# Optimization experiments

Measured on AMD Instinct MI355X. Metric: run time of the kernel, lower is better.

## Reference

```python
import jax, jax.numpy as jnp
import numpy as np

B, T, D, H = 512, 200, 64, 256
C1, C2, C3, R1 = 1024, 256, 10, 1024

def _lin(k, out_d, in_d):
    k1, k2 = jax.random.split(k)
    lim = 1.0 / np.sqrt(in_d)
    w = jax.random.uniform(k1, (out_d, in_d), minval=-lim, maxval=lim, dtype=jnp.float32)
    b = jax.random.uniform(k2, (out_d,), minval=-lim, maxval=lim, dtype=jnp.float32)
    return w, b

def setup_inputs() -> dict:
    key = jax.random.key(0)
    ks = jax.random.split(key, 12)
    lim = 1.0 / np.sqrt(H)
    u = lambda k, sh: jax.random.uniform(k, sh, minval=-lim, maxval=lim, dtype=jnp.float32)
    inp = {"x": jax.random.normal(ks[0], (B, T, D), dtype=jnp.float32)}
    # LSTM layer 0 (input dim D) and layer 1 (input dim H); torch gate order i,f,g,o
    inp["W_ih0"], inp["b_ih0"], inp["b_hh0"] = u(ks[1], (4 * H, D)), u(ks[2], (4 * H,)), u(ks[3], (4 * H,))
    inp["W_ih1"], inp["b_ih1"], inp["b_hh1"] = u(ks[4], (4 * H, H)), u(ks[5], (4 * H,)), u(ks[6], (4 * H,))
    inp["fc1_w"], inp["fc1_b"] = _lin(ks[7], C1, H * T)
    inp["fc2_w"], inp["fc2_b"] = _lin(ks[8], C2, C1)
    inp["fc3_w"], inp["fc3_b"] = _lin(ks[9], C3, C2)
    inp["fc4_w"], inp["fc4_b"] = _lin(ks[10], R1, H * T)
    inp["fc5_w"], inp["fc5_b"] = _lin(ks[11], T, R1)
    return inp

def _lstm_step_zero(x, W_ih, b_ih, b_hh):
    # Single LSTM cell step from h0=c0=0, applied independently to every
    # (batch, timestep) position: gates = x @ W_ih^T + b_ih + b_hh
    gates = jnp.einsum('btd,gd->btg', x, W_ih) + b_ih + b_hh  # [B,T,4H]
    i, f, g, o = jnp.split(gates, 4, axis=-1)  # torch gate order i,f,g,o
    c = jax.nn.sigmoid(i) * jnp.tanh(g)        # c0 = 0 => forget gate irrelevant
    return jax.nn.sigmoid(o) * jnp.tanh(c)

def reference(x, W_ih0, b_ih0, b_hh0, W_ih1, b_ih1, b_hh1,
              fc1_w, fc1_b, fc2_w, fc2_b, fc3_w, fc3_b,
              fc4_w, fc4_b, fc5_w, fc5_b):
    h0 = _lstm_step_zero(x, W_ih0, b_ih0, b_hh0)          # [B,T,H]
    out_total = _lstm_step_zero(h0, W_ih1, b_ih1, b_hh1)  # [B,T,H]
    flat = out_total.reshape(-1, H * T)
    # classification head (dropout = identity in eval)
    c = jax.nn.relu(flat @ fc1_w.T + fc1_b)
    c = jax.nn.relu(c @ fc2_w.T + fc2_b)
    output_class3 = c @ fc3_w.T + fc3_b                   # [B,C3]
    r = jax.nn.relu(flat @ fc4_w.T + fc4_b)
    output_reg3 = (r @ fc5_w.T + fc5_b).reshape(-1, T, 1) # [B,T,1]
    return (out_total, output_class3, output_reg3)
```

## Files before the change

kernel.cpp:

```cpp
#include <hip/hip_runtime.h>
#include <hip/hip_bf16.h>

typedef unsigned short u16;
typedef unsigned int   u32;

typedef __bf16 bf16x8 __attribute__((ext_vector_type(8)));
typedef float  f32x4  __attribute__((ext_vector_type(4)));

__device__ __forceinline__ bf16x8 as_bf16x8(uint4 u) {
    return __builtin_bit_cast(bf16x8, u);
}

__device__ __forceinline__ u16 bf16r(float f) {
    return (u16)((__float_as_uint(f) + 0x8000u) >> 16);
}
__device__ __forceinline__ u32 pack2(float lo, float hi) {
    u32 a = __float_as_uint(lo) + 0x8000u;
    u32 b = __float_as_uint(hi) + 0x8000u;
    return (a >> 16) | (b & 0xFFFF0000u);
}

__device__ __forceinline__ u32 cvtpk(float lo, float hi) {
    u32 r;
    asm("v_cvt_pk_bf16_f32 %0, %1, %2" : "=v"(r) : "v"(lo), "v"(hi));
    return r;
}
__device__ __forceinline__ bf16x8 wcvt(float4 a, float4 b) {
    uint4 u;
    u.x = cvtpk(a.x, a.y); u.y = cvtpk(a.z, a.w);
    u.z = cvtpk(b.x, b.y); u.w = cvtpk(b.z, b.w);
    return as_bf16x8(u);
}

__device__ __forceinline__ float sigmoidf_(float x) {
    return 1.0f / (1.0f + __expf(-x));
}
__device__ __forceinline__ float tanhf_(float x) {
    float xx = fminf(fmaxf(x, -15.0f), 15.0f);
    float e = __expf(2.0f * xx);
    return (e - 1.0f) / (e + 1.0f);
}

__global__ __launch_bounds__(256) void prep_kernel(
    const float* __restrict__ W_ih0, const float* __restrict__ b_ih0, const float* __restrict__ b_hh0,
    const float* __restrict__ W_ih1, const float* __restrict__ b_ih1, const float* __restrict__ b_hh1,
    u16* __restrict__ Wb0, u16* __restrict__ Wb1, float* __restrict__ bs0, float* __restrict__ bs1)
{
    int idx = blockIdx.x * 256 + threadIdx.x;
    if (idx < 49152) {
        int k = idx & 63, sn = idx >> 6;
        int n = sn & 255, s = sn >> 8;
        int row = (s == 0) ? n : (s == 1 ? 512 + n : 768 + n);
        Wb0[idx] = bf16r(W_ih0[row * 64 + k]);
    } else if (idx < 245760) {
        int j = idx - 49152;
        int k = j & 255, sn = j >> 8;
        int n = sn & 255, s = sn >> 8;
        int row = (s == 0) ? n : (s == 1 ? 512 + n : 768 + n);
        Wb1[j] = bf16r(W_ih1[row * 256 + k]);
    } else if (idx < 247296) {
        int j = idx - 245760;
        int l = j / 768, q = j - l * 768;
        int s = q >> 8, n = q & 255;
        int row = (s == 0) ? n : (s == 1 ? 512 + n : 768 + n);
        if (l == 0) bs0[q] = b_ih0[row] + b_hh0[row];
        else        bs1[q] = b_ih1[row] + b_hh1[row];
    }
}

template<int K, bool IS_L1>
__global__ __launch_bounds__(256) void lstm_kernel(
    const void* __restrict__ xin,
    const u16*  __restrict__ Wb,
    const float* __restrict__ bsum,
    u16*   __restrict__ hout_b,
    float* __restrict__ hout_f)
{
    constexpr int SP = K + 8;
    __shared__ u16 x_s[64 * SP];
    const int t  = threadIdx.x;
    const int m0 = blockIdx.y * 64;
    const int n0 = blockIdx.x * 64;

    if (!IS_L1) {
        const float* xf = (const float*)xin;
        int row = t >> 2, seg = t & 3;
        const float* src = xf + (size_t)(m0 + row) * 64 + seg * 16;
        u32 p0 = pack2(src[0],  src[1]);
        u32 p1 = pack2(src[2],  src[3]);
        u32 p2 = pack2(src[4],  src[5]);
        u32 p3 = pack2(src[6],  src[7]);
        u32 p4 = pack2(src[8],  src[9]);
        u32 p5 = pack2(src[10], src[11]);
        u32 p6 = pack2(src[12], src[13]);
        u32 p7 = pack2(src[14], src[15]);
        u16* dst = x_s + row * SP + seg * 16;
        *(uint4*)(dst)     = make_uint4(p0, p1, p2, p3);
        *(uint4*)(dst + 8) = make_uint4(p4, p5, p6, p7);
    } else {
        const u16* xb = (const u16*)xin;
        #pragma unroll
        for (int p = 0; p < 2; p++) {
            int row = p * 32 + (t >> 3);
            int seg = t & 7;
            const u16* src = xb + (size_t)(m0 + row) * 256 + seg * 32;
            u16* dst = x_s + row * SP + seg * 32;
            #pragma unroll
            for (int i = 0; i < 4; i++)
                *(uint4*)(dst + i * 8) = *(const uint4*)(src + i * 8);
        }
    }
    __syncthreads();

    const int lane = t & 63, w = t >> 6, quad = lane >> 4, l15 = lane & 15;
    const int n = n0 + w * 16 + l15;

    f32x4 acc[3][4] = {};
    #pragma unroll
    for (int kc = 0; kc < K; kc += 32) {
        bf16x8 b[3];
        #pragma unroll
        for (int s = 0; s < 3; s++)
            b[s] = as_bf16x8(*(const uint4*)(Wb + (size_t)(s * 256 + n) * K + kc + quad * 8));
        #pragma unroll
        for (int mt = 0; mt < 4; mt++) {
            bf16x8 a = as_bf16x8(*(const uint4*)(x_s + (mt * 16 + l15) * SP + kc + quad * 8));
            #pragma unroll
            for (int s = 0; s < 3; s++)
                acc[s][mt] = __builtin_amdgcn_mfma_f32_16x16x32_bf16(a, b[s], acc[s][mt], 0, 0, 0);
        }
    }

    const float bi = bsum[n], bg = bsum[256 + n], bo = bsum[512 + n];
    #pragma unroll
    for (int mt = 0; mt < 4; mt++) {
        #pragma unroll
        for (int r = 0; r < 4; r++) {
            int m = m0 + mt * 16 + quad * 4 + r;
            float vi = acc[0][mt][r] + bi;
            float vg = acc[1][mt][r] + bg;
            float vo = acc[2][mt][r] + bo;
            float c  = sigmoidf_(vi) * tanhf_(vg);
            float h  = sigmoidf_(vo) * tanhf_(c);
            size_t off = (size_t)m * 256 + n;
            if (IS_L1) { hout_f[off] = h; hout_b[off] = bf16r(h); }
            else       { hout_b[off] = bf16r(h); }
        }
    }
}

__global__ __launch_bounds__(256) void fc14_kernel(
    const u16* __restrict__ flat,
    const float* __restrict__ w1, const float* __restrict__ w4,
    float* __restrict__ P)
{
    __shared__ __align__(16) u16 A_s[128 * 128];
    const int t  = threadIdx.x;
    const int nb = blockIdx.x;
    const int mb = blockIdx.y, z = blockIdx.z;
    const int m0 = mb * 128;
    const float* W = (nb < 16) ? w1 : w4;
    const int wrow0 = (nb & 15) * 64;

    const int lane = t & 63, w = t >> 6;
    const int quad = lane >> 4, l15 = lane & 15;
    const int wm = w >> 1, wn = w & 1;
    const int xk = l15 & 7;

    const int rlo = lane >> 4;
    const int s16 = lane & 15;
    const int colA = s16 ^ rlo;
    const int colB = s16 ^ (4 | rlo);
    const u16* fsrc = flat + (size_t)(m0 + w * 32 + rlo) * 51200 + (size_t)z * 6400;

    const float* wb0 = W + (size_t)(wrow0 + wn * 32 +  0 + l15) * 51200 + (size_t)z * 6400 + quad * 8;
    const float* wb1 = W + (size_t)(wrow0 + wn * 32 + 16 + l15) * 51200 + (size_t)z * 6400 + quad * 8;

    f32x4 acc[4][2] = {};

    for (int kg = 0; kg < 50; kg++) {
        const int kk = kg * 128;
        __syncthreads();
        #pragma unroll
        for (int it = 0; it < 8; it++) {
            const u16* src = fsrc + (size_t)(it * 4) * 51200 + kk
                           + ((it & 1) ? colB : colA) * 8;
            u16* dst = A_s + (w * 8 + it) * 512;
            __builtin_amdgcn_global_load_lds(
                (const __attribute__((address_space(1))) u16*)src,
                (__attribute__((address_space(3))) u16*)dst, 16, 0, 0);
        }
        float4 wf[4][2][2];
        #pragma unroll
        for (int c = 0; c < 4; c++) {
            wf[c][0][0] = *(const float4*)(wb0 + kk + c * 32);
            wf[c][0][1] = *(const float4*)(wb0 + kk + c * 32 + 4);
            wf[c][1][0] = *(const float4*)(wb1 + kk + c * 32);
            wf[c][1][1] = *(const float4*)(wb1 + kk + c * 32 + 4);
        }
        __syncthreads();
        #pragma unroll
        for (int c = 0; c < 4; c++) {
            bf16x8 b0 = wcvt(wf[c][0][0], wf[c][0][1]);
            bf16x8 b1 = wcvt(wf[c][1][0], wf[c][1][1]);
            const int soff = ((c * 4 + quad) ^ xk) * 8;
            #pragma unroll
            for (int mt = 0; mt < 4; mt++) {
                const int row = wm * 64 + mt * 16 + l15;
                bf16x8 a = as_bf16x8(*(const uint4*)(A_s + row * 128 + soff));
                acc[mt][0] = __builtin_amdgcn_mfma_f32_16x16x32_bf16(a, b0, acc[mt][0], 0, 0, 0);
                acc[mt][1] = __builtin_amdgcn_mfma_f32_16x16x32_bf16(a, b1, acc[mt][1], 0, 0, 0);
            }
        }
    }

    float* Pp = P + (size_t)z * (512 * 2048);
    #pragma unroll
    for (int mt = 0; mt < 4; mt++) {
        #pragma unroll
        for (int nt = 0; nt < 2; nt++) {
            const int ng = nb * 64 + wn * 32 + nt * 16 + l15;
            #pragma unroll
            for (int r = 0; r < 4; r++) {
                const int m = m0 + wm * 64 + mt * 16 + quad * 4 + r;
                Pp[(size_t)m * 2048 + ng] = acc[mt][nt][r];
            }
        }
    }
}

__global__ __launch_bounds__(256) void reduce_bias_relu(
    const float* __restrict__ P, const float* __restrict__ b1, const float* __restrict__ b4,
    float* __restrict__ c1r)
{
    int idx = blockIdx.x * 256 + threadIdx.x;
    int m = idx >> 9;
    int n = (idx & 511) * 4;
    float4 s = make_float4(0.f, 0.f, 0.f, 0.f);
    #pragma unroll
    for (int z = 0; z < 8; z++) {
        float4 p = *(const float4*)(P + ((size_t)z * 512 + m) * 2048 + n);
        s.x += p.x; s.y += p.y; s.z += p.z; s.w += p.w;
    }
    const float* bp = (n < 1024) ? (b1 + n) : (b4 + (n - 1024));
    float4 b = *(const float4*)bp;
    s.x = fmaxf(s.x + b.x, 0.f);
    s.y = fmaxf(s.y + b.y, 0.f);
    s.z = fmaxf(s.z + b.z, 0.f);
    s.w = fmaxf(s.w + b.w, 0.f);
    *(float4*)(c1r + (size_t)m * 2048 + n) = s;
}

__global__ __launch_bounds__(256) void sgemm_small(
    const float* __restrict__ A, int lda,
    const float* __restrict__ W,
    const float* __restrict__ bias,
    float* __restrict__ out, int ldo,
    int M, int N, int K, int do_relu)
{
    __shared__ float As[16 * 260];
    const int t = threadIdx.x;
    const int m0 = blockIdx.y * 16, n0 = blockIdx.x * 16;
    const int mi = t >> 4, ni = t & 15;
    const int n = n0 + ni;
    const bool act = n < N;
    float acc = 0.f;
    for (int kc = 0; kc < K; kc += 256) {
        __syncthreads();
        {
            int row = t >> 4, cb = (t & 15) * 16;
            const float* src = A + (size_t)(m0 + row) * lda + kc + cb;
            float* dst = As + row * 260 + cb;
            *(float4*)(dst)      = *(const float4*)(src);
            *(float4*)(dst + 4)  = *(const float4*)(src + 4);
            *(float4*)(dst + 8)  = *(const float4*)(src + 8);
            *(float4*)(dst + 12) = *(const float4*)(src + 12);
        }
        __syncthreads();
        if (act) {
            const float* wr = W + (size_t)n * K + kc;
            const float* ar = As + mi * 260;
            #pragma unroll 4
            for (int k = 0; k < 256; k += 4) {
                float4 w4 = *(const float4*)(wr + k);
                float4 a4 = *(const float4*)(ar + k);
                acc += a4.x * w4.x + a4.y * w4.y + a4.z * w4.z + a4.w * w4.w;
            }
        }
    }
    if (act) {
        float v = acc + bias[n];
        if (do_relu) v = fmaxf(v, 0.f);
        out[(size_t)(m0 + mi) * ldo + n] = v;
    }
}

extern "C" void kernel_launch(void* const* d_in, const int* in_sizes, int n_in,
                              void* d_out, int out_size, void* d_ws, size_t ws_size,
                              hipStream_t stream) {
    const float* x      = (const float*)d_in[0];
    const float* W_ih0  = (const float*)d_in[1];
    const float* b_ih0  = (const float*)d_in[2];
    const float* b_hh0  = (const float*)d_in[3];
    const float* W_ih1  = (const float*)d_in[4];
    const float* b_ih1  = (const float*)d_in[5];
    const float* b_hh1  = (const float*)d_in[6];
    const float* fc1_w  = (const float*)d_in[7];
    const float* fc1_b  = (const float*)d_in[8];
    const float* fc2_w  = (const float*)d_in[9];
    const float* fc2_b  = (const float*)d_in[10];
    const float* fc3_w  = (const float*)d_in[11];
    const float* fc3_b  = (const float*)d_in[12];
    const float* fc4_w  = (const float*)d_in[13];
    const float* fc4_b  = (const float*)d_in[14];
    const float* fc5_w  = (const float*)d_in[15];
    const float* fc5_b  = (const float*)d_in[16];
    float* out = (float*)d_out;

    char* ws = (char*)d_ws;
    u16*   Wb0  = (u16*)  (ws + 0);
    u16*   Wb1  = (u16*)  (ws + 98304);
    float* bs0  = (float*)(ws + 491520);
    float* bs1  = (float*)(ws + 494592);
    u16*   h0   = (u16*)  (ws + 524288);
    float* P    = (float*)(ws + 524288);
    u16*   flat = (u16*)  (ws + 52953088);
    float* c1r  = (float*)(ws + 105381888);
    float* c2   = (float*)(ws + 109576192);
    if (ws_size < 110100480) return;

    prep_kernel<<<966, 256, 0, stream>>>(W_ih0, b_ih0, b_hh0, W_ih1, b_ih1, b_hh1,
                                         Wb0, Wb1, bs0, bs1);
    lstm_kernel<64,  false><<<dim3(4, 1600), 256, 0, stream>>>(x,  Wb0, bs0, h0,   nullptr);
    lstm_kernel<256, true ><<<dim3(4, 1600), 256, 0, stream>>>(h0, Wb1, bs1, flat, out);
    fc14_kernel<<<dim3(32, 4, 8), 256, 0, stream>>>(flat, fc1_w, fc4_w, P);
    reduce_bias_relu<<<1024, 256, 0, stream>>>(P, fc1_b, fc4_b, c1r);
    sgemm_small<<<dim3(16, 32), 256, 0, stream>>>(c1r,        2048, fc2_w, fc2_b, c2,             256, 512, 256, 1024, 1);
    sgemm_small<<<dim3(13, 32), 256, 0, stream>>>(c1r + 1024, 2048, fc5_w, fc5_b, out + 26219520, 200, 512, 200, 1024, 0);
    sgemm_small<<<dim3(1,  32), 256, 0, stream>>>(c2,          256, fc3_w, fc3_b, out + 26214400,  10, 512,  10,  256, 0);
}
```

Baseline: 1.168 ms.

## Double-buffer fc1/fc4 GEMM LDS tiles and weight registers across k-steps

Splits the fc14 kernel's shared-memory A tile into two buffers and keeps two sets of weight registers. The next k-slice's async global-to-LDS loads and fp32 weight loads are issued before computing on the current slice, so memory latency can overlap with the MFMA work. The trade is double the LDS (64KB per block) and more registers, which may lower occupancy.

```diff
diff --git a/kernel.cpp b/kernel.cpp
--- a/kernel.cpp
+++ b/kernel.cpp
@@ -154,7 +154,7 @@
     const float* __restrict__ w1, const float* __restrict__ w4,
     float* __restrict__ P)
 {
-    __shared__ __align__(16) u16 A_s[128 * 128];
+    __shared__ __align__(16) u16 A_s[2][128 * 128];
     const int t  = threadIdx.x;
     const int nb = blockIdx.x;
     const int mb = blockIdx.y, z = blockIdx.z;
@@ -177,42 +177,65 @@
     const float* wb1 = W + (size_t)(wrow0 + wn * 32 + 16 + l15) * 51200 + (size_t)z * 6400 + quad * 8;
 
     f32x4 acc[4][2] = {};
-
-    for (int kg = 0; kg < 50; kg++) {
-        const int kk = kg * 128;
+    float4 wf0[4][2][2];
+    float4 wf1[4][2][2];
+
+#define STAGE(BUF, KK) do {                                                    \
+    _Pragma("unroll")                                                          \
+    for (int it = 0; it < 8; it++) {                                           \
+        const u16* src_ = fsrc + (size_t)(it * 4) * 51200 + (KK)               \
+                        + ((it & 1) ? colB : colA) * 8;                        \
+        u16* dst_ = A_s[BUF] + (w * 8 + it) * 512;                             \
+        __builtin_amdgcn_global_load_lds(                                      \
+            (const __attribute__((address_space(1))) u16*)src_,                \
+            (__attribute__((address_space(3))) u16*)dst_, 16, 0, 0);           \
+    } } while (0)
+
+#define LOADW(WF, KK) do {                                                     \
+    _Pragma("unroll")                                                          \
+    for (int c_ = 0; c_ < 4; c_++) {                                           \
+        WF[c_][0][0] = *(const float4*)(wb0 + (KK) + c_ * 32);                 \
+        WF[c_][0][1] = *(const float4*)(wb0 + (KK) + c_ * 32 + 4);             \
+        WF[c_][1][0] = *(const float4*)(wb1 + (KK) + c_ * 32);                 \
+        WF[c_][1][1] = *(const float4*)(wb1 + (KK) + c_ * 32 + 4);             \
+    } } while (0)
+
+#define COMPUTE(BUF, WF) do {                                                  \
+    _Pragma("unroll")                                                          \
+    for (int c_ = 0; c_ < 4; c_++) {                                           \
+        bf16x8 b0_ = wcvt(WF[c_][0][0], WF[c_][0][1]);                         \
+        bf16x8 b1_ = wcvt(WF[c_][1][0], WF[c_][1][1]);                         \
+        const int soff_ = ((c_ * 4 + quad) ^ xk) * 8;                          \
+        _Pragma("unroll")                                                      \
+        for (int mt_ = 0; mt_ < 4; mt_++) {                                    \
+            const int row_ = wm * 64 + mt_ * 16 + l15;                         \
+            bf16x8 a_ = as_bf16x8(*(const uint4*)(A_s[BUF] + row_ * 128 + soff_)); \
+            acc[mt_][0] = __builtin_amdgcn_mfma_f32_16x16x32_bf16(a_, b0_, acc[mt_][0], 0, 0, 0); \
+            acc[mt_][1] = __builtin_amdgcn_mfma_f32_16x16x32_bf16(a_, b1_, acc[mt_][1], 0, 0, 0); \
+        }                                                                      \
+    } } while (0)
+
+    STAGE(0, 0);
+    LOADW(wf0, 0);
+    __syncthreads();
+
+    for (int kg = 0; kg < 50; kg += 2) {
+        const int kkE = kg * 128;
+        STAGE(1, kkE + 128);
+        LOADW(wf1, kkE + 128);
+        COMPUTE(0, wf0);
         __syncthreads();
-        #pragma unroll
-        for (int it = 0; it < 8; it++) {
-            const u16* src = fsrc + (size_t)(it * 4) * 51200 + kk
-                           + ((it & 1) ? colB : colA) * 8;
-            u16* dst = A_s + (w * 8 + it) * 512;
-            __builtin_amdgcn_global_load_lds(
-                (const __attribute__((address_space(1))) u16*)src,
-                (__attribute__((address_space(3))) u16*)dst, 16, 0, 0);
-        }
-        float4 wf[4][2][2];
-        #pragma unroll
-        for (int c = 0; c < 4; c++) {
-            wf[c][0][0] = *(const float4*)(wb0 + kk + c * 32);
-            wf[c][0][1] = *(const float4*)(wb0 + kk + c * 32 + 4);
-            wf[c][1][0] = *(const float4*)(wb1 + kk + c * 32);
-            wf[c][1][1] = *(const float4*)(wb1 + kk + c * 32 + 4);
-        }
+        if (kg + 2 < 50) {
+            STAGE(0, kkE + 256);
+            LOADW(wf0, kkE + 256);
+        }
+        COMPUTE(1, wf1);
         __syncthreads();
-        #pragma unroll
-        for (int c = 0; c < 4; c++) {
-            bf16x8 b0 = wcvt(wf[c][0][0], wf[c][0][1]);
-            bf16x8 b1 = wcvt(wf[c][1][0], wf[c][1][1]);
-            const int soff = ((c * 4 + quad) ^ xk) * 8;
-            #pragma unroll
-            for (int mt = 0; mt < 4; mt++) {
-                const int row = wm * 64 + mt * 16 + l15;
-                bf16x8 a = as_bf16x8(*(const uint4*)(A_s + row * 128 + soff));
-                acc[mt][0] = __builtin_amdgcn_mfma_f32_16x16x32_bf16(a, b0, acc[mt][0], 0, 0, 0);
-                acc[mt][1] = __builtin_amdgcn_mfma_f32_16x16x32_bf16(a, b1, acc[mt][1], 0, 0, 0);
-            }
-        }
-    }
+    }
+
+#undef STAGE
+#undef LOADW
+#undef COMPUTE
 
     float* Pp = P + (size_t)z * (512 * 2048);
     #pragma unroll
```

New measurement: 1.194 ms. +2.3%, slower.
